# Kernel optimization log

Measured on AMD Instinct MI355X. Metric: run time of the kernel, lower is better.

The kernel has to match this reference:

```python
import jax, jax.numpy as jnp
import numpy as np

PS = 8          # patch_size
NF = 64         # num_feat
HEADS = 1
HW = 64         # hard-coded spatial size (Fold output_size=(64,64))
DIM = PS * PS * NF          # 4096
HID = DIM // HEADS          # 4096
NPATCH = (HW // PS) ** 2    # 64


def conv2d(x, w, b, groups=1):
    # x: [N,C,H,W], w: [O, C//groups, 3, 3], padding=1 stride=1 == SAME
    y = jax.lax.conv_general_dilated(
        x, w, window_strides=(1, 1), padding='SAME',
        dimension_numbers=('NCHW', 'OIHW', 'NCHW'),
        feature_group_count=groups)
    return y + b[None, :, None, None]


def unfold(x):
    # nn.Unfold(kernel=PS, stride=PS): [N,C,64,64] -> [N, C*PS*PS, NPATCH]
    N, C = x.shape[0], x.shape[1]
    g = HW // PS
    x = x.reshape(N, C, g, PS, g, PS)          # [N,C,gh,pi,gw,pj]
    x = x.transpose(0, 1, 3, 5, 2, 4)          # [N,C,pi,pj,gh,gw]
    return x.reshape(N, C * PS * PS, g * g)


def fold(y):
    # nn.Fold(output=(64,64), kernel=PS, stride=PS): inverse of unfold (non-overlapping)
    N = y.shape[0]
    g = HW // PS
    y = y.reshape(N, NF, PS, PS, g, g)         # [N,C,pi,pj,gh,gw]
    y = y.transpose(0, 1, 4, 2, 5, 3)          # [N,C,gh,pi,gw,pj]
    return y.reshape(N, NF, HW, HW)


def setup_inputs() -> dict:
    key = jax.random.key(0)
    ks = jax.random.split(key, 9)
    b, t = 4, 16
    x = jax.random.normal(ks[0], (b, t, NF, HW, HW), dtype=jnp.float32)
    s_dw = 1.0 / np.sqrt(9.0)          # depthwise: fan_in = 1*3*3
    s_fc = 1.0 / np.sqrt(NF * 9.0)     # full conv: fan_in = 64*3*3
    qw = jax.random.normal(ks[1], (NF, 1, 3, 3), jnp.float32) * s_dw
    qb = jax.random.normal(ks[2], (NF,), jnp.float32) * 0.01
    kw = jax.random.normal(ks[3], (NF, 1, 3, 3), jnp.float32) * s_dw
    kb = jax.random.normal(ks[4], (NF,), jnp.float32) * 0.01
    vw = jax.random.normal(ks[5], (NF, NF, 3, 3), jnp.float32) * s_fc
    vb = jax.random.normal(ks[6], (NF,), jnp.float32) * 0.01
    cw = jax.random.normal(ks[7], (NF, NF, 3, 3), jnp.float32) * s_fc
    cb = jax.random.normal(ks[8], (NF,), jnp.float32) * 0.01
    return {"x": x, "qw": qw, "qb": qb, "kw": kw, "kb": kb,
            "vw": vw, "vb": vb, "cw": cw, "cb": cb}


def reference(x, qw, qb, kw, kb, vw, vb, cw, cb):
    b, t, c, h, w = x.shape
    H, d, n = HEADS, HID, NPATCH
    xf = x.reshape(b * t, c, h, w)
    q = conv2d(xf, qw, qb, groups=NF)   # depthwise
    k = conv2d(xf, kw, kb, groups=NF)   # depthwise
    v = conv2d(xf, vw, vb)              # full conv
    # unfold -> [b,t,H,d,n] -> [b,H,d,t*n]
    def to_tokens(z):
        z = unfold(z).reshape(b, t, H, d, n)
        return z.transpose(0, 2, 3, 1, 4).reshape(b, H, d, t * n)
    uq, uk, uv = to_tokens(q), to_tokens(k), to_tokens(v)
    attn = jnp.einsum('bhdi,bhdj->bhij', uq, uk) * (d ** -0.5)
    attn = jax.nn.softmax(attn, axis=-1)
    ax = jnp.einsum('bhij,bhdj->bhid', attn, uv)          # [b,H,t*n,d]
    ax = ax.reshape(b, H, t, n, d).transpose(0, 2, 1, 4, 3)  # [b,t,H,d,n]
    ax = ax.reshape(b * t, DIM, n)
    feat = fold(ax)                                        # [b*t,C,64,64]
    out = conv2d(feat, cw, cb).reshape(x.shape)
    return out + x
```

## Files before the change

### kernel.cpp

```cpp
#include <hip/hip_runtime.h>

typedef unsigned short u16;
typedef unsigned int   u32;

typedef __bf16 bf16_t;
typedef bf16_t bf16x8 __attribute__((ext_vector_type(8)));
typedef float  f32x4  __attribute__((ext_vector_type(4)));

__device__ __forceinline__ float bf2f(u16 h) { return __uint_as_float(((u32)h) << 16); }
__device__ __forceinline__ u16 f2bf(float f) {
    u32 u = __float_as_uint(f);
    u32 r = u + 0x7fffu + ((u >> 16) & 1u);
    return (u16)(r >> 16);
}
__device__ __forceinline__ void unpack2(u32 v, float& a, float& b) {
    a = __uint_as_float(v << 16);
    b = __uint_as_float(v & 0xffff0000u);
}


__global__ __launch_bounds__(256) void dwconv_qk(
    const float* __restrict__ x, const float* __restrict__ qw, const float* __restrict__ qb,
    const float* __restrict__ kw, const float* __restrict__ kb,
    u16* __restrict__ qtok, u16* __restrict__ ktok)
{
    __shared__ float ts[64][65];
    int img = blockIdx.x >> 6, c = blockIdx.x & 63;
    int tid = threadIdx.x;
    const float* xp = x + ((size_t)((img << 6) + c) << 12);
    #pragma unroll
    for (int i = 0; i < 4; i++) {
        int p = i * 1024 + tid * 4;
        int r = p >> 6, col = p & 63;
        float4 v = *(const float4*)(xp + p);
        ts[r][col] = v.x; ts[r][col + 1] = v.y; ts[r][col + 2] = v.z; ts[r][col + 3] = v.w;
    }
    float qwv[9], kwv[9];
    #pragma unroll
    for (int i = 0; i < 9; i++) { qwv[i] = qw[c * 9 + i]; kwv[i] = kw[c * 9 + i]; }
    float qbb = qb[c], kbb = kb[c];
    __syncthreads();

    int r = tid >> 2, q = tid & 3;
    int b = img >> 4, t = img & 15;
    int gh = r >> 3, pr = r & 7;
    size_t base = (((size_t)(b << 10) + (t << 6) + (gh << 3)) << 12) + (c << 6) + (pr << 3);

    #pragma unroll
    for (int s = 0; s < 2; s++) {
        int gw = q * 2 + s, w0 = gw << 3;
        float qa[8], ka[8];
        #pragma unroll
        for (int i = 0; i < 8; i++) { qa[i] = qbb; ka[i] = kbb; }
        #pragma unroll
        for (int ky = 0; ky < 3; ky++) {
            int hh = r + ky - 1;
            if (hh < 0 || hh > 63) continue;
            float xr[10];
            #pragma unroll
            for (int cc = 0; cc < 10; cc++) {
                int ww = w0 - 1 + cc;
                xr[cc] = (ww < 0 || ww > 63) ? 0.f : ts[hh][ww];
            }
            #pragma unroll
            for (int kx = 0; kx < 3; kx++) {
                float wq = qwv[ky * 3 + kx], wk = kwv[ky * 3 + kx];
                #pragma unroll
                for (int i = 0; i < 8; i++) {
                    qa[i] += xr[i + kx] * wq;
                    ka[i] += xr[i + kx] * wk;
                }
            }
        }
        union { u16 h8[8]; uint4 u; } pq, pk;
        #pragma unroll
        for (int i = 0; i < 8; i++) { pq.h8[i] = f2bf(qa[i]); pk.h8[i] = f2bf(ka[i]); }
        size_t o = base + ((size_t)gw << 12);
        *(uint4*)&qtok[o] = pq.u;
        *(uint4*)&ktok[o] = pk.u;
    }
}

__global__ __launch_bounds__(256) void nchw_to_nhwc(
    const float* __restrict__ x, u16* __restrict__ xb)
{
    __shared__ float ts[64][65];
    int img = blockIdx.x >> 6, h = blockIdx.x & 63;
    int tid = threadIdx.x;
    const float* xp = x + ((size_t)img << 18) + (h << 6);
    int c = tid >> 2, wg = (tid & 3) << 4;
    #pragma unroll
    for (int i = 0; i < 4; i++) {
        float4 v = *(const float4*)(xp + ((size_t)c << 12) + wg + i * 4);
        ts[c][wg + i * 4 + 0] = v.x; ts[c][wg + i * 4 + 1] = v.y;
        ts[c][wg + i * 4 + 2] = v.z; ts[c][wg + i * 4 + 3] = v.w;
    }
    __syncthreads();
    int w = tid >> 2, cg = (tid & 3) << 4;
    union { u16 h8[8]; uint4 u; } p0, p1;
    #pragma unroll
    for (int m = 0; m < 8; m++) {
        p0.h8[m] = f2bf(ts[cg + m][w]);
        p1.h8[m] = f2bf(ts[cg + 8 + m][w]);
    }
    u16* dst = xb + (((((size_t)img << 6) + h) << 6) + w) * 64 + cg;
    *(uint4*)dst       = p0.u;
    *(uint4*)(dst + 8) = p1.u;
}

__global__ __launch_bounds__(256) void weight_prep2(
    const float* __restrict__ vw, const float* __restrict__ cw, u16* __restrict__ wt)
{
    int e = blockIdx.x * 256 + threadIdx.x;
    if (e >= 73728) return;
    int half = e >= 36864;
    int e2 = e - (half ? 36864 : 0);
    int tap = e2 >> 12, rem = e2 & 4095, cout = rem >> 6, cin = rem & 63;
    const float* src = half ? cw : vw;
    wt[e] = f2bf(src[((cout << 6) + cin) * 9 + tap]);
}

template<bool IS_C>
__global__ __launch_bounds__(256, 2) void conv_mfma(
    const u16* __restrict__ xb, const u16* __restrict__ wt,
    const float* __restrict__ bias, const float* __restrict__ xres,
    u16* __restrict__ vt, float* __restrict__ out)
{
    __shared__ u16 xs[21120];

    int tid = threadIdx.x, lane = tid & 63, wv = tid >> 6;
    int img = blockIdx.x >> 3, rowblk = blockIdx.x & 7;
    int h0 = rowblk << 3;
    int r16 = lane & 15, kb = lane >> 4;

    const uint4 z4 = make_uint4(0, 0, 0, 0);
    for (int i = tid; i < 80; i += 256) {
        int r = i >> 3, cs = i & 7;
        int col = (cs & 1) ? 65 : 0, slot = cs >> 1;
        *(uint4*)&xs[(r * 66 + col) * 32 + slot * 8] = z4;
    }
    if (rowblk == 0)
        for (int i = tid; i < 264; i += 256)
            *(uint4*)&xs[(i >> 2) * 32 + (i & 3) * 8] = z4;
    if (rowblk == 7)
        for (int i = tid; i < 264; i += 256)
            *(uint4*)&xs[(9 * 66 + (i >> 2)) * 32 + (i & 3) * 8] = z4;

    int boff[8];
    #pragma unroll
    for (int nf = 0; nf < 8; nf++)
        boff[nf] = (((wv << 1) + (nf >> 2)) * 66 + (nf & 3) * 16 + r16) * 32 + kb * 8;

    const u16* xb_i  = xb + ((size_t)img << 18);
    const u16* wfrag = wt + (kb << 3);

    f32x4 acc[4][8] = {};

    for (int c0 = 0; c0 < 64; c0 += 32) {
        __syncthreads();
        #pragma unroll
        for (int r = 0; r < 10; r++) {
            int h = h0 + r - 1;
            if (h < 0 || h > 63) continue;
            const u16* src = xb_i + (size_t)(((h << 6) + (wv << 4) + (lane >> 2)) << 6)
                             + c0 + ((lane & 3) << 3);
            u16* dst = xs + (r * 66 + 1 + (wv << 4)) * 32;
            __builtin_amdgcn_global_load_lds(
                (const __attribute__((address_space(1))) u32*)src,
                (__attribute__((address_space(3))) u32*)dst, 16, 0, 0);
        }
        __syncthreads();

        #pragma unroll
        for (int tap = 0; tap < 9; tap++) {
            int toffX = ((tap / 3) * 66 + (tap % 3)) * 32;
            bf16x8 af[4];
            #pragma unroll
            for (int m = 0; m < 4; m++)
                af[m] = *(const bf16x8*)(wfrag + (size_t)(((tap << 6) + (m << 4) + r16) << 6) + c0);
            #pragma unroll
            for (int nf = 0; nf < 8; nf++) {
                bf16x8 bv = *(const bf16x8*)&xs[toffX + boff[nf]];
                #pragma unroll
                for (int m = 0; m < 4; m++)
                    acc[m][nf] = __builtin_amdgcn_mfma_f32_16x16x32_bf16(
                        af[m], bv, acc[m][nf], 0, 0, 0);
            }
        }
    }

    int b = img >> 4, t = img & 15;
    if constexpr (!IS_C) {
        __syncthreads();
        u16* wbuf = xs + (wv << 12);
        int j0 = (t << 6) + (rowblk << 3);
        #pragma unroll
        for (int mh = 0; mh < 2; mh++) {
            #pragma unroll
            for (int mm = 0; mm < 2; mm++) {
                int m = mh * 2 + mm;
                #pragma unroll
                for (int q = 0; q < 4; q++) {
                    int cm = mm * 16 + (kb << 2) + q;
                    float bvs = bias[mh * 32 + cm];
                    #pragma unroll
                    for (int nf = 0; nf < 8; nf++) {
                        int lrL = nf >> 2;
                        int pc  = r16 & 7;
                        int gw  = ((nf & 3) << 1) | (r16 >> 3);
                        wbuf[(((cm << 1) | lrL) << 6) + (pc << 3) + gw] =
                            f2bf(acc[m][nf][q] + bvs);
                    }
                }
            }
            #pragma unroll
            for (int it = 0; it < 8; it++) {
                int cid = it * 64 + lane;
                int cm  = cid >> 4;
                int lrL = (cid >> 3) & 1;
                int pc  = cid & 7;
                int lr  = (wv << 1) | lrL;
                int cout = mh * 32 + cm;
                int dd  = (((lr << 3) | pc) << 6) | cout;
                uint4 val = *(uint4*)&wbuf[cid << 3];
                *(uint4*)&vt[(((size_t)((b << 12) + dd)) << 10) + j0] = val;
            }
            if (mh == 0) __syncthreads();
        }
    } else {
        #pragma unroll
        for (int m = 0; m < 4; m++) {
            #pragma unroll
            for (int q = 0; q < 4; q++) {
                int cout = (m << 4) + (kb << 2) + q;
                float bvs = bias[cout];
                #pragma unroll
                for (int nf = 0; nf < 8; nf++) {
                    int lr = (wv << 1) + (nf >> 2);
                    int w = (nf & 3) * 16 + r16;
                    int h = h0 + lr;
                    size_t o = ((size_t)((img << 6) + cout) << 12) + (h << 6) + w;
                    out[o] = acc[m][nf][q] + bvs + xres[o];
                }
            }
        }
    }
}

template<int TM, int LDA, int LDB, int LDC, int KTOT, int MT, int NT, int EPI>
__global__ __launch_bounds__(256, 3) void mfma_abt(
    const u16* __restrict__ Ag, const u16* __restrict__ Bg,
    const float* __restrict__ invl, u16* __restrict__ Cg)
{
    constexpr int MF = TM / 32;
    __shared__ u16 As[TM * 64];
    __shared__ u16 Bs[128 * 64];

    int tid  = threadIdx.x;
    int lane = tid & 63, wv = tid >> 6;
    int nt   = blockIdx.x % NT;
    int rest = blockIdx.x / NT;
    int mt   = rest % MT;
    int bi   = rest / MT;

    const u16* Ab = Ag + (size_t)bi * (1024 * (size_t)LDA) + (size_t)(mt * TM) * LDA;
    const u16* Bb = Bg + (size_t)bi * ((size_t)NT * 128 * LDB) + (size_t)(nt * 128) * LDB;

    int srow = tid >> 3;
    int slot = tid & 7;
    int wr = wv >> 1, wc = wv & 1;
    int r16 = lane & 15, kb = lane >> 4;

    f32x4 acc[MF][4] = {};

    for (int k0 = 0; k0 < KTOT; k0 += 64) {
        __syncthreads();
        #pragma unroll
        for (int it = 0; it < MF; it++) {
            int rl = it * 32 + srow;
            int kg = slot ^ (rl & 7);
            const u16* sa = Ab + (size_t)rl * LDA + k0 + kg * 8;
            u16* da = As + it * 2048 + wv * 512;
            __builtin_amdgcn_global_load_lds(
                (const __attribute__((address_space(1))) u32*)sa,
                (__attribute__((address_space(3))) u32*)da, 16, 0, 0);
        }
        #pragma unroll
        for (int it = 0; it < 4; it++) {
            int rl = it * 32 + srow;
            int kg = slot ^ (rl & 7);
            const u16* sb = Bb + (size_t)rl * LDB + k0 + kg * 8;
            u16* db = Bs + it * 2048 + wv * 512;
            __builtin_amdgcn_global_load_lds(
                (const __attribute__((address_space(1))) u32*)sb,
                (__attribute__((address_space(3))) u32*)db, 16, 0, 0);
        }
        __syncthreads();

        #pragma unroll
        for (int kk = 0; kk < 2; kk++) {
            bf16x8 af[MF], bfr[4];
            #pragma unroll
            for (int m = 0; m < MF; m++) {
                int row  = wr * (TM / 2) + m * 16 + r16;
                int boff = row * 128 + (((kk * 32 + kb * 8) * 2) ^ ((row & 7) << 4));
                af[m] = *(const bf16x8*)((const char*)As + boff);
            }
            #pragma unroll
            for (int n = 0; n < 4; n++) {
                int row  = wc * 64 + n * 16 + r16;
                int boff = row * 128 + (((kk * 32 + kb * 8) * 2) ^ ((row & 7) << 4));
                bfr[n] = *(const bf16x8*)((const char*)Bs + boff);
            }
            #pragma unroll
            for (int m = 0; m < MF; m++)
                #pragma unroll
                for (int n = 0; n < 4; n++)
                    acc[m][n] = __builtin_amdgcn_mfma_f32_16x16x32_bf16(
                        af[m], bfr[n], acc[m][n], 0, 0, 0);
        }
    }

    size_t crow0 = (size_t)bi * 1024 + (size_t)mt * TM + wr * (TM / 2);
    int col0 = nt * 128 + wc * 64;
    #pragma unroll
    for (int m = 0; m < MF; m++) {
        float il[4] = {1.f, 1.f, 1.f, 1.f};
        if constexpr (EPI == 2) {
            #pragma unroll
            for (int q = 0; q < 4; q++)
                il[q] = invl[crow0 + m * 16 + kb * 4 + q];
        }
        #pragma unroll
        for (int n = 0; n < 4; n++) {
            #pragma unroll
            for (int q = 0; q < 4; q++) {
                int i_loc = m * 16 + kb * 4 + q;
                int j     = col0 + n * 16 + r16;
                float v   = acc[m][n][q];
                if constexpr (EPI == 0) {
                    Cg[(crow0 + i_loc) * (size_t)LDC + j] = f2bf(__expf(v * 0.015625f));
                } else {
                    int i2 = mt * TM + wr * (TM / 2) + i_loc;
                    int t = i2 >> 6, patch = i2 & 63;
                    int c = j & 63, pr = (j >> 9) & 7, pc = (j >> 6) & 7;
                    int h = ((patch >> 3) << 3) + pr, w2 = ((patch & 7) << 3) + pc;
                    size_t o = ((((size_t)(bi * 16 + t) << 6) + h) << 6) + w2;
                    Cg[(o << 6) + c] = f2bf(v * il[q]);
                }
            }
        }
    }
}

__global__ __launch_bounds__(256) void rowsum_inv_kernel(
    const u16* __restrict__ p, float* __restrict__ invl)
{
    int row = blockIdx.x, tid = threadIdx.x;
    uint2 v = ((const uint2*)(p + ((size_t)row << 10)))[tid];
    float a, b, c, d;
    unpack2(v.x, a, b); unpack2(v.y, c, d);
    float s = (a + b) + (c + d);
    #pragma unroll
    for (int off = 32; off; off >>= 1) s += __shfl_xor(s, off);
    __shared__ float rs[4];
    if ((tid & 63) == 0) rs[tid >> 6] = s;
    __syncthreads();
    if (tid == 0) invl[row] = 1.f / ((rs[0] + rs[1]) + (rs[2] + rs[3]));
}

extern "C" void kernel_launch(void* const* d_in, const int* in_sizes, int n_in,
                              void* d_out, int out_size, void* d_ws, size_t ws_size,
                              hipStream_t stream)
{
    const float* x  = (const float*)d_in[0];
    const float* qw = (const float*)d_in[1];
    const float* qb = (const float*)d_in[2];
    const float* kw = (const float*)d_in[3];
    const float* kb = (const float*)d_in[4];
    const float* vw = (const float*)d_in[5];
    const float* vb = (const float*)d_in[6];
    const float* cw = (const float*)d_in[7];
    const float* cb = (const float*)d_in[8];
    float* out = (float*)d_out;

    char* ws = (char*)d_ws;
    u16*   qtok  = (u16*)d_out;
    u16*   ktok  = (u16*)ws;
    u16*   probs = (u16*)(ws + (size_t)32 * 1024 * 1024);
    float* invl  = (float*)(ws + (size_t)40 * 1024 * 1024);
    u16*   wtv   = (u16*)(ws + (size_t)40 * 1024 * 1024 + 65536);
    u16*   wtc   = wtv + 36864;
    u16*   xbuf  = ktok;
    u16*   vt    = qtok;
    u16*   axb   = ktok;

    weight_prep2<<<288, 256, 0, stream>>>(vw, cw, wtv);

    dwconv_qk<<<4096, 256, 0, stream>>>(x, qw, qb, kw, kb, qtok, ktok);

    mfma_abt<64, 4096, 4096, 1024, 4096, 16, 8, 0><<<512, 256, 0, stream>>>(
        qtok, ktok, nullptr, probs);

    rowsum_inv_kernel<<<4096, 256, 0, stream>>>(probs, invl);

    nchw_to_nhwc<<<4096, 256, 0, stream>>>(x, xbuf);

    conv_mfma<false><<<512, 256, 0, stream>>>(xbuf, wtv, vb, nullptr, vt, nullptr);

    mfma_abt<128, 1024, 1024, 4096, 1024, 8, 32, 2><<<1024, 256, 0, stream>>>(
        probs, vt, invl, axb);

    conv_mfma<true><<<512, 256, 0, stream>>>(axb, wtc, cb, x, nullptr, out);
}
```

Measured before the change: 349.7 us.

## Restructure conv MFMA kernel to 8 waves with one output row each

The 3x3 conv MFMA kernel now runs with 512 threads (8 waves), each wave computing one output row instead of two. This halves the per-wave accumulator count and raises occupancy, to hide latency better. It also changes the LDS layout of the input tile (16-pixel groups with channel-sliced 8-element segments and separate halo slots), aiming to cut bank conflicts on B-fragment reads. The cost is that every wave reloads the weight fragments for its row, and the epilogue has to be reindexed for the new layout.

```diff
diff --git a/kernel.cpp b/kernel.cpp
--- a/kernel.cpp
+++ b/kernel.cpp
@@ -121,7 +121,7 @@
 }
 
 template<bool IS_C>
-__global__ __launch_bounds__(256, 2) void conv_mfma(
+__global__ __launch_bounds__(512, 4) void conv_mfma(
     const u16* __restrict__ xb, const u16* __restrict__ wt,
     const float* __restrict__ bias, const float* __restrict__ xres,
     u16* __restrict__ vt, float* __restrict__ out)
@@ -134,65 +134,80 @@
     int r16 = lane & 15, kb = lane >> 4;
 
     const uint4 z4 = make_uint4(0, 0, 0, 0);
-    for (int i = tid; i < 80; i += 256) {
-        int r = i >> 3, cs = i & 7;
-        int col = (cs & 1) ? 65 : 0, slot = cs >> 1;
-        *(uint4*)&xs[(r * 66 + col) * 32 + slot * 8] = z4;
+    for (int i = tid; i < 80; i += 512) {
+        int r = i >> 3, k = i & 7;
+        *(uint4*)&xs[r * 2112 + 2048 + (k >> 2) * 32 + (k & 3) * 8] = z4;
     }
     if (rowblk == 0)
-        for (int i = tid; i < 264; i += 256)
-            *(uint4*)&xs[(i >> 2) * 32 + (i & 3) * 8] = z4;
+        for (int i = tid; i < 264; i += 512) *(uint4*)&xs[i * 8] = z4;
     if (rowblk == 7)
-        for (int i = tid; i < 264; i += 256)
-            *(uint4*)&xs[(9 * 66 + (i >> 2)) * 32 + (i & 3) * 8] = z4;
-
-    int boff[8];
-    #pragma unroll
-    for (int nf = 0; nf < 8; nf++)
-        boff[nf] = (((wv << 1) + (nf >> 2)) * 66 + (nf & 3) * 16 + r16) * 32 + kb * 8;
+        for (int i = tid; i < 264; i += 512) *(uint4*)&xs[9 * 2112 + i * 8] = z4;
+
+    int pxoff[4][3];
+    #pragma unroll
+    for (int g = 0; g < 4; g++) {
+        #pragma unroll
+        for (int dx = 0; dx < 3; dx++) {
+            int cc = g * 16 + r16 + dx - 1;
+            int off;
+            if (cc < 0)        off = 2048 + kb * 8;
+            else if (cc >= 64) off = 2080 + kb * 8;
+            else               off = (cc >> 4) * 512 + kb * 128 + (cc & 15) * 8;
+            pxoff[g][dx] = off;
+        }
+    }
 
     const u16* xb_i  = xb + ((size_t)img << 18);
     const u16* wfrag = wt + (kb << 3);
 
-    f32x4 acc[4][8] = {};
+    f32x4 acc[4][4] = {};
 
     for (int c0 = 0; c0 < 64; c0 += 32) {
         __syncthreads();
         #pragma unroll
-        for (int r = 0; r < 10; r++) {
+        for (int k = 0; k < 5; k++) {
+            int i = wv + k * 8;
+            int r = i >> 2, g = i & 3;
             int h = h0 + r - 1;
-            if (h < 0 || h > 63) continue;
-            const u16* src = xb_i + (size_t)(((h << 6) + (wv << 4) + (lane >> 2)) << 6)
-                             + c0 + ((lane & 3) << 3);
-            u16* dst = xs + (r * 66 + 1 + (wv << 4)) * 32;
-            __builtin_amdgcn_global_load_lds(
-                (const __attribute__((address_space(1))) u32*)src,
-                (__attribute__((address_space(3))) u32*)dst, 16, 0, 0);
+            if (h >= 0 && h < 64) {
+                const u16* src = xb_i + (size_t)(((h << 6) + (g << 4) + r16) << 6)
+                                 + c0 + (kb << 3);
+                u16* dst = xs + r * 2112 + g * 512;
+                __builtin_amdgcn_global_load_lds(
+                    (const __attribute__((address_space(1))) u32*)src,
+                    (__attribute__((address_space(3))) u32*)dst, 16, 0, 0);
+            }
         }
         __syncthreads();
 
         #pragma unroll
-        for (int tap = 0; tap < 9; tap++) {
-            int toffX = ((tap / 3) * 66 + (tap % 3)) * 32;
-            bf16x8 af[4];
-            #pragma unroll
-            for (int m = 0; m < 4; m++)
-                af[m] = *(const bf16x8*)(wfrag + (size_t)(((tap << 6) + (m << 4) + r16) << 6) + c0);
-            #pragma unroll
-            for (int nf = 0; nf < 8; nf++) {
-                bf16x8 bv = *(const bf16x8*)&xs[toffX + boff[nf]];
+        for (int dy = 0; dy < 3; dy++) {
+            int rowb = (wv + dy) * 2112;
+            #pragma unroll
+            for (int dx = 0; dx < 3; dx++) {
+                int tap = dy * 3 + dx;
+                bf16x8 af[4];
                 #pragma unroll
                 for (int m = 0; m < 4; m++)
-                    acc[m][nf] = __builtin_amdgcn_mfma_f32_16x16x32_bf16(
-                        af[m], bv, acc[m][nf], 0, 0, 0);
-            }
-        }
-    }
-
-    int b = img >> 4, t = img & 15;
+                    af[m] = *(const bf16x8*)(wfrag
+                              + (size_t)(((tap << 6) + (m << 4) + r16) << 6) + c0);
+                #pragma unroll
+                for (int g = 0; g < 4; g++) {
+                    bf16x8 bv = *(const bf16x8*)&xs[rowb + pxoff[g][dx]];
+                    #pragma unroll
+                    for (int m = 0; m < 4; m++)
+                        acc[m][g] = __builtin_amdgcn_mfma_f32_16x16x32_bf16(
+                            af[m], bv, acc[m][g], 0, 0, 0);
+                }
+            }
+        }
+    }
+
+    int h = h0 + wv;
     if constexpr (!IS_C) {
         __syncthreads();
-        u16* wbuf = xs + (wv << 12);
+        u16* wbuf = xs + (wv << 11);
+        int b = img >> 4, t = img & 15;
         int j0 = (t << 6) + (rowblk << 3);
         #pragma unroll
         for (int mh = 0; mh < 2; mh++) {
@@ -201,31 +216,24 @@
                 int m = mh * 2 + mm;
                 #pragma unroll
                 for (int q = 0; q < 4; q++) {
-                    int cm = mm * 16 + (kb << 2) + q;
-                    float bvs = bias[mh * 32 + cm];
+                    int cm = (mm << 4) + (kb << 2) + q;
+                    float bvs = bias[(mh << 5) + cm];
                     #pragma unroll
-                    for (int nf = 0; nf < 8; nf++) {
-                        int lrL = nf >> 2;
-                        int pc  = r16 & 7;
-                        int gw  = ((nf & 3) << 1) | (r16 >> 3);
-                        wbuf[(((cm << 1) | lrL) << 6) + (pc << 3) + gw] =
-                            f2bf(acc[m][nf][q] + bvs);
+                    for (int g = 0; g < 4; g++) {
+                        int w = (g << 4) + r16;
+                        int pc = w & 7, gw = w >> 3;
+                        wbuf[((cm << 3) + pc) * 8 + gw] = f2bf(acc[m][g][q] + bvs);
                     }
                 }
             }
             #pragma unroll
-            for (int it = 0; it < 8; it++) {
-                int cid = it * 64 + lane;
-                int cm  = cid >> 4;
-                int lrL = (cid >> 3) & 1;
-                int pc  = cid & 7;
-                int lr  = (wv << 1) | lrL;
-                int cout = mh * 32 + cm;
-                int dd  = (((lr << 3) | pc) << 6) | cout;
+            for (int it = 0; it < 4; it++) {
+                int cid = (it << 6) + lane;
+                int cm = cid >> 3, pc = cid & 7;
+                int dd = ((wv << 3) + pc) * 64 + (mh << 5) + cm;
                 uint4 val = *(uint4*)&wbuf[cid << 3];
                 *(uint4*)&vt[(((size_t)((b << 12) + dd)) << 10) + j0] = val;
             }
-            if (mh == 0) __syncthreads();
         }
     } else {
         #pragma unroll
@@ -235,12 +243,10 @@
                 int cout = (m << 4) + (kb << 2) + q;
                 float bvs = bias[cout];
                 #pragma unroll
-                for (int nf = 0; nf < 8; nf++) {
-                    int lr = (wv << 1) + (nf >> 2);
-                    int w = (nf & 3) * 16 + r16;
-                    int h = h0 + lr;
+                for (int g = 0; g < 4; g++) {
+                    int w = (g << 4) + r16;
                     size_t o = ((size_t)((img << 6) + cout) << 12) + (h << 6) + w;
-                    out[o] = acc[m][nf][q] + bvs + xres[o];
+                    out[o] = acc[m][g][q] + bvs + xres[o];
                 }
             }
         }
@@ -406,10 +412,10 @@
 
     nchw_to_nhwc<<<4096, 256, 0, stream>>>(x, xbuf);
 
-    conv_mfma<false><<<512, 256, 0, stream>>>(xbuf, wtv, vb, nullptr, vt, nullptr);
+    conv_mfma<false><<<512, 512, 0, stream>>>(xbuf, wtv, vb, nullptr, vt, nullptr);
 
     mfma_abt<128, 1024, 1024, 4096, 1024, 8, 32, 2><<<1024, 256, 0, stream>>>(
         probs, vt, invl, axb);
 
-    conv_mfma<true><<<512, 256, 0, stream>>>(axb, wtc, cb, x, nullptr, out);
-}
+    conv_mfma<true><<<512, 512, 0, stream>>>(axb, wtc, cb, x, nullptr, out);
+}
```

Result: slower. 400.6 us (+14.6%).

## Stage conv weights in LDS and reorganize input tile layout for conflict-free reads

Applied to the files above, without the earlier changes.

Weight fragments for the MFMA conv are now staged into a per-block LDS buffer via async global-to-LDS loads instead of being read from global memory per tap. The weight prep kernel reorders the bf16 weights into k-group-major order to match, and the input tile LDS layout is changed to a k-group-interleaved format with separate halo slots, using precomputed per-column offsets. This aims to cut redundant global weight traffic and LDS bank conflicts. It adds about 36 KB of LDS per block, which may lower occupancy below the two-blocks-per-CU launch bound.

```diff
diff --git a/kernel.cpp b/kernel.cpp
--- a/kernel.cpp
+++ b/kernel.cpp
@@ -115,7 +115,11 @@
     if (e >= 73728) return;
     int half = e >= 36864;
     int e2 = e - (half ? 36864 : 0);
-    int tap = e2 >> 12, rem = e2 & 4095, cout = rem >> 6, cin = rem & 63;
+    int tap = e2 >> 12;
+    int kbg = (e2 >> 9) & 7;
+    int cout = (e2 >> 3) & 63;
+    int s = e2 & 7;
+    int cin = (kbg << 3) + s;
     const float* src = half ? cw : vw;
     wt[e] = f2bf(src[((cout << 6) + cin) * 9 + tap]);
 }
@@ -127,6 +131,7 @@
     u16* __restrict__ vt, float* __restrict__ out)
 {
     __shared__ u16 xs[21120];
+    __shared__ u16 wl[18432];
 
     int tid = threadIdx.x, lane = tid & 63, wv = tid >> 6;
     int img = blockIdx.x >> 3, rowblk = blockIdx.x & 7;
@@ -135,56 +140,77 @@
 
     const uint4 z4 = make_uint4(0, 0, 0, 0);
     for (int i = tid; i < 80; i += 256) {
-        int r = i >> 3, cs = i & 7;
-        int col = (cs & 1) ? 65 : 0, slot = cs >> 1;
-        *(uint4*)&xs[(r * 66 + col) * 32 + slot * 8] = z4;
+        int r = i >> 3, k = i & 7;
+        *(uint4*)&xs[r * 2112 + 2048 + k * 8] = z4;
     }
     if (rowblk == 0)
-        for (int i = tid; i < 264; i += 256)
-            *(uint4*)&xs[(i >> 2) * 32 + (i & 3) * 8] = z4;
+        for (int i = tid; i < 264; i += 256) *(uint4*)&xs[i * 8] = z4;
     if (rowblk == 7)
-        for (int i = tid; i < 264; i += 256)
-            *(uint4*)&xs[(9 * 66 + (i >> 2)) * 32 + (i & 3) * 8] = z4;
-
-    int boff[8];
-    #pragma unroll
-    for (int nf = 0; nf < 8; nf++)
-        boff[nf] = (((wv << 1) + (nf >> 2)) * 66 + (nf & 3) * 16 + r16) * 32 + kb * 8;
-
-    const u16* xb_i  = xb + ((size_t)img << 18);
-    const u16* wfrag = wt + (kb << 3);
+        for (int i = tid; i < 264; i += 256) *(uint4*)&xs[9 * 2112 + i * 8] = z4;
+
+    int pxoff[4][3];
+    #pragma unroll
+    for (int g = 0; g < 4; g++) {
+        #pragma unroll
+        for (int dx = 0; dx < 3; dx++) {
+            int cc = g * 16 + r16 + dx - 1;
+            int off;
+            if (cc < 0)        off = 2048 + kb * 8;
+            else if (cc >= 64) off = 2080 + kb * 8;
+            else               off = (cc >> 4) * 512 + kb * 128 + (cc & 15) * 8;
+            pxoff[g][dx] = off;
+        }
+    }
+
+    const u16* xb_i = xb + ((size_t)img << 18);
 
     f32x4 acc[4][8] = {};
 
     for (int c0 = 0; c0 < 64; c0 += 32) {
         __syncthreads();
         #pragma unroll
-        for (int r = 0; r < 10; r++) {
+        for (int k = 0; k < 10; k++) {
+            int i = wv + (k << 2);
+            int r = i >> 2, g = i & 3;
             int h = h0 + r - 1;
-            if (h < 0 || h > 63) continue;
-            const u16* src = xb_i + (size_t)(((h << 6) + (wv << 4) + (lane >> 2)) << 6)
-                             + c0 + ((lane & 3) << 3);
-            u16* dst = xs + (r * 66 + 1 + (wv << 4)) * 32;
+            if (h >= 0 && h < 64) {
+                const u16* src = xb_i + (size_t)(((h << 6) + (g << 4) + r16) << 6)
+                                 + c0 + (kb << 3);
+                u16* dst = xs + r * 2112 + g * 512;
+                __builtin_amdgcn_global_load_lds(
+                    (const __attribute__((address_space(1))) u32*)src,
+                    (__attribute__((address_space(3))) u32*)dst, 16, 0, 0);
+            }
+        }
+        #pragma unroll
+        for (int tp = 0; tp < 9; tp++) {
+            const u16* srcw = wt + tp * 4096 + (c0 << 6) + tid * 8;
+            u16* dstw = wl + tp * 2048 + (wv << 9);
             __builtin_amdgcn_global_load_lds(
-                (const __attribute__((address_space(1))) u32*)src,
-                (__attribute__((address_space(3))) u32*)dst, 16, 0, 0);
+                (const __attribute__((address_space(1))) u32*)srcw,
+                (__attribute__((address_space(3))) u32*)dstw, 16, 0, 0);
         }
         __syncthreads();
 
         #pragma unroll
-        for (int tap = 0; tap < 9; tap++) {
-            int toffX = ((tap / 3) * 66 + (tap % 3)) * 32;
-            bf16x8 af[4];
-            #pragma unroll
-            for (int m = 0; m < 4; m++)
-                af[m] = *(const bf16x8*)(wfrag + (size_t)(((tap << 6) + (m << 4) + r16) << 6) + c0);
-            #pragma unroll
-            for (int nf = 0; nf < 8; nf++) {
-                bf16x8 bv = *(const bf16x8*)&xs[toffX + boff[nf]];
+        for (int dy = 0; dy < 3; dy++) {
+            #pragma unroll
+            for (int dx = 0; dx < 3; dx++) {
+                int tap = dy * 3 + dx;
+                bf16x8 af[4];
                 #pragma unroll
                 for (int m = 0; m < 4; m++)
-                    acc[m][nf] = __builtin_amdgcn_mfma_f32_16x16x32_bf16(
-                        af[m], bv, acc[m][nf], 0, 0, 0);
+                    af[m] = *(const bf16x8*)&wl[tap * 2048 + (kb << 9)
+                                                + (((m << 4) + r16) << 3)];
+                #pragma unroll
+                for (int nf = 0; nf < 8; nf++) {
+                    int rowb = ((wv << 1) + (nf >> 2) + dy) * 2112;
+                    bf16x8 bv = *(const bf16x8*)&xs[rowb + pxoff[nf & 3][dx]];
+                    #pragma unroll
+                    for (int m = 0; m < 4; m++)
+                        acc[m][nf] = __builtin_amdgcn_mfma_f32_16x16x32_bf16(
+                            af[m], bv, acc[m][nf], 0, 0, 0);
+                }
             }
         }
     }
```

Result: faster. 320.6 us (-8.3%).
